# Performance work log

Measured on AMD Instinct MI355X. Metric: run time of the kernel, lower is better.

The kernel has to match this reference:

```python
import jax, jax.numpy as jnp
import numpy as np

D_MODEL = 1024
N_HEADS = 16
HEAD_DIM = D_MODEL // N_HEADS
D_FF = 4 * D_MODEL
EPS = 1e-5


def layer_norm(x, gamma, beta):
    mu = jnp.mean(x, axis=-1, keepdims=True)
    var = jnp.var(x, axis=-1, keepdims=True)
    return (x - mu) * jax.lax.rsqrt(var + EPS) * gamma + beta


def setup_inputs() -> dict:
    key = jax.random.key(0)
    ks = jax.random.split(key, 12)
    B, T, S = 4, 2048, 2048
    s_in = 1.0 / np.sqrt(D_MODEL)
    s_ff = 1.0 / np.sqrt(D_FF)
    return {
        "x": jax.random.normal(ks[0], (B, T, D_MODEL), jnp.float32),
        "context": jax.random.normal(ks[1], (B, S, D_MODEL), jnp.float32),
        "Wq": jax.random.normal(ks[2], (D_MODEL, D_MODEL), jnp.float32) * s_in,
        "Wk": jax.random.normal(ks[3], (D_MODEL, D_MODEL), jnp.float32) * s_in,
        "Wv": jax.random.normal(ks[4], (D_MODEL, D_MODEL), jnp.float32) * s_in,
        "Wo": jax.random.normal(ks[5], (D_MODEL, D_MODEL), jnp.float32) * s_in,
        "W1": jax.random.normal(ks[6], (D_FF, D_MODEL), jnp.float32) * s_in,
        "W2": jax.random.normal(ks[7], (D_MODEL, D_FF), jnp.float32) * s_ff,
        "g1": jnp.ones((D_MODEL,), jnp.float32),
        "b1": jnp.zeros((D_MODEL,), jnp.float32),
        "gc": jnp.ones((D_MODEL,), jnp.float32),
        "bc": jnp.zeros((D_MODEL,), jnp.float32),
        "g2": jnp.ones((D_MODEL,), jnp.float32),
        "b2": jnp.zeros((D_MODEL,), jnp.float32),
    }


def reference(x, context, Wq, Wk, Wv, Wo, W1, W2, g1, b1, gc, bc, g2, b2):
    B, T, C = x.shape
    S = context.shape[1]
    residual = x
    xn = layer_norm(x, g1, b1)
    cn = layer_norm(context, gc, bc)
    # torch Linear: y = x @ W.T ; split heads -> [B, H, T, Dh]
    q = (xn @ Wq.T).reshape(B, T, N_HEADS, HEAD_DIM).transpose(0, 2, 1, 3)
    k = (cn @ Wk.T).reshape(B, S, N_HEADS, HEAD_DIM).transpose(0, 2, 1, 3)
    v = (cn @ Wv.T).reshape(B, S, N_HEADS, HEAD_DIM).transpose(0, 2, 1, 3)
    scale = HEAD_DIM ** (-0.5)
    attn = jax.nn.softmax(jnp.einsum('bhtd,bhsd->bhts', q, k) * scale, axis=-1)
    o = jnp.einsum('bhts,bhsd->bhtd', attn, v).transpose(0, 2, 1, 3).reshape(B, T, C)
    x = residual + o @ Wo.T
    residual = x
    h = layer_norm(x, g2, b2)
    h = jax.nn.gelu(h @ W1.T, approximate=False) @ W2.T
    return residual + h
```

## Files before the change

### kernel.cpp

```cpp
#include <hip/hip_runtime.h>
#include <cstdint>
#include <cstddef>

typedef __attribute__((ext_vector_type(8))) short short8;
typedef __attribute__((ext_vector_type(4))) short short4v;
typedef __attribute__((ext_vector_type(4))) float f32x4;
typedef __attribute__((ext_vector_type(4))) unsigned uint4v;

#define DEV static __device__ __forceinline__

DEV short f2bf(float f) {
    unsigned u = __builtin_bit_cast(unsigned, f);
    unsigned r = (u + 0x7fffu + ((u >> 16) & 1u)) >> 16;
    return (short)r;
}

DEV unsigned cvt_pk_bf16(float a, float b) {
    unsigned r;
    asm("v_cvt_pk_bf16_f32 %0, %1, %2" : "=v"(r) : "v"(a), "v"(b));
    return r;
}

DEV float exp2_hw(float x) {
    float r;
    asm("v_exp_f32 %0, %1" : "=v"(r) : "v"(x));
    return r;
}

DEV float rcp_hw(float x) {
    float r;
    asm("v_rcp_f32 %0, %1" : "=v"(r) : "v"(x));
    return r;
}

DEV float gelu_f(float v) {
    float t  = v * (1.0f + 0.044715f * v * v);
    float e  = exp2_hw(fminf(2.3022082f * t, 126.0f));
    return v * e * rcp_hw(e + 1.0f);
}

DEV void gld16(const void* g, void* l) {
    __builtin_amdgcn_global_load_lds((const __attribute__((address_space(1))) void*)g,
                                     (__attribute__((address_space(3))) void*)l, 16, 0, 0);
}

#define MFMA(c, a, b) asm volatile("v_mfma_f32_16x16x32_bf16 %0, %1, %2, %0" : "+v"(c) : "v"(a), "v"(b))
#define BAR() asm volatile("s_barrier" ::: "memory")

__global__ __launch_bounds__(256) void cvt_weights(
    const float* __restrict__ wq, const float* __restrict__ wk,
    const float* __restrict__ wv, const float* __restrict__ wo,
    const float* __restrict__ w1, const float* __restrict__ w2,
    short* __restrict__ dst) {
    long long gid = (long long)blockIdx.x * 256 + threadIdx.x;
    long long i4 = gid * 4;
    const float* src; long long loc;
    if (i4 < (4LL << 20)) {
        int s = (int)(i4 >> 20);
        src = (s == 0) ? wq : (s == 1) ? wk : (s == 2) ? wv : wo;
        loc = i4 & ((1LL << 20) - 1);
    } else {
        long long r = i4 - (4LL << 20);
        int s = (int)(r >> 22);
        src = s ? w2 : w1;
        loc = r & ((1LL << 22) - 1);
    }
    float4 v = *(const float4*)(src + loc);
    short4v o;
    o.x = f2bf(v.x); o.y = f2bf(v.y); o.z = f2bf(v.z); o.w = f2bf(v.w);
    *(short4v*)(dst + i4) = o;
}

__global__ __launch_bounds__(256) void ln_bf16(const float* __restrict__ x,
                                               const float* __restrict__ g,
                                               const float* __restrict__ bt,
                                               short* __restrict__ out) {
    int row = blockIdx.x;
    const float4* xr = (const float4*)(x + (size_t)row * 1024);
    float4 v = xr[threadIdx.x];
    float s  = v.x + v.y + v.z + v.w;
    float s2 = v.x*v.x + v.y*v.y + v.z*v.z + v.w*v.w;
    #pragma unroll
    for (int m = 1; m < 64; m <<= 1) { s += __shfl_xor(s, m); s2 += __shfl_xor(s2, m); }
    __shared__ float red[8];
    int wid = threadIdx.x >> 6;
    if ((threadIdx.x & 63) == 0) { red[wid] = s; red[4 + wid] = s2; }
    __syncthreads();
    s  = red[0] + red[1] + red[2] + red[3];
    s2 = red[4] + red[5] + red[6] + red[7];
    float mu  = s * (1.0f / 1024.0f);
    float var = fmaxf(s2 * (1.0f / 1024.0f) - mu * mu, 0.0f);
    float rs  = rsqrtf(var + 1e-5f);
    float4 gv = ((const float4*)g)[threadIdx.x];
    float4 bv = ((const float4*)bt)[threadIdx.x];
    short4v o;
    o.x = f2bf((v.x - mu) * rs * gv.x + bv.x);
    o.y = f2bf((v.y - mu) * rs * gv.y + bv.y);
    o.z = f2bf((v.z - mu) * rs * gv.z + bv.z);
    o.w = f2bf((v.w - mu) * rs * gv.w + bv.w);
    *(short4v*)(out + (size_t)row * 1024 + (size_t)threadIdx.x * 4) = o;
}

template<int MODE>
DEV void gemm_core(const short* __restrict__ A, const short* __restrict__ B,
                   void* __restrict__ out, const float* __restrict__ resid,
                   int N, int K, int lda, int ldb, float osc, int bm, int bn) {
    __shared__ short lds[2 * 32768];
    const int tid = threadIdx.x;
    const int row0 = bm << 8, col0 = bn << 8;
    const int wid = tid >> 6, lane = tid & 63;
    const int wm = wid >> 2, wn = wid & 3;
    const int lr = lane & 15, lg = lane >> 4;
    const int NK = K >> 6;

    auto stage = [&](int kt, int which) {
        int d = kt & 1;
        const short* src; int rb; int ld;
        if (which < 2) { src = A; rb = row0; ld = lda; } else { src = B; rb = col0; ld = ldb; }
        int rhalf = (which & 1) << 7;
        short* dst = lds + d * 32768 + which * 8192;
        #pragma unroll
        for (int l = 0; l < 2; ++l) {
            int g = l * 512 + tid;
            int r = g >> 3, c = g & 7;
            gld16(src + (size_t)(rb + rhalf + r) * ld + kt * 64 + ((c ^ (r & 7)) << 3),
                  dst + g * 8);
        }
    };

    f32x4 acc[8][4] = {};

    stage(0, 0); stage(0, 1); stage(0, 2); stage(0, 3);
    if (NK > 1) {
        stage(1, 2); stage(1, 3);
        asm volatile("s_waitcnt vmcnt(4)" ::: "memory");
    } else {
        asm volatile("s_waitcnt vmcnt(0)" ::: "memory");
    }
    BAR();

    const int rBbase = (wn & 1) << 6;
    for (int t = 0; t < NK; ++t) {
        const short* bufA = lds + (t & 1) * 32768 + wm * 8192;
        const short* bufB = lds + (t & 1) * 32768 + 16384 + (wn >> 1) * 8192;
        bool st1 = (t + 1) < NK, st2 = (t + 2) < NK;
        short8 bf2[2][4];

        {
            short8 af[4];
            #pragma unroll
            for (int i = 0; i < 4; ++i) {
                int r = i * 16 + lr;
                af[i] = *(const short8*)(bufA + r * 64 + ((lg ^ (r & 7)) << 3));
            }
            #pragma unroll
            for (int j = 0; j < 4; ++j) {
                int rB = rBbase + j * 16 + lr;
                bf2[0][j] = *(const short8*)(bufB + rB * 64 + ((lg ^ (rB & 7)) << 3));
            }
            if (st1) stage(t + 1, 0);
            BAR();
            __builtin_amdgcn_s_setprio(1);
            #pragma unroll
            for (int i = 0; i < 4; ++i)
                #pragma unroll
                for (int j = 0; j < 4; ++j)
                    MFMA(acc[i][j], af[i], bf2[0][j]);
            __builtin_amdgcn_s_setprio(0);
            BAR();
        }
        {
            short8 af[4];
            #pragma unroll
            for (int i = 0; i < 4; ++i) {
                int r = i * 16 + lr;
                af[i] = *(const short8*)(bufA + r * 64 + (((4 + lg) ^ (r & 7)) << 3));
            }
            #pragma unroll
            for (int j = 0; j < 4; ++j) {
                int rB = rBbase + j * 16 + lr;
                bf2[1][j] = *(const short8*)(bufB + rB * 64 + (((4 + lg) ^ (rB & 7)) << 3));
            }
            if (st1) stage(t + 1, 1);
            BAR();
            __builtin_amdgcn_s_setprio(1);
            #pragma unroll
            for (int i = 0; i < 4; ++i)
                #pragma unroll
                for (int j = 0; j < 4; ++j)
                    MFMA(acc[i][j], af[i], bf2[1][j]);
            __builtin_amdgcn_s_setprio(0);
            BAR();
        }
        {
            short8 af[4];
            #pragma unroll
            for (int i = 0; i < 4; ++i) {
                int r = 64 + i * 16 + lr;
                af[i] = *(const short8*)(bufA + r * 64 + ((lg ^ (r & 7)) << 3));
            }
            if (st2) stage(t + 2, 2);
            BAR();
            __builtin_amdgcn_s_setprio(1);
            #pragma unroll
            for (int i = 0; i < 4; ++i)
                #pragma unroll
                for (int j = 0; j < 4; ++j)
                    MFMA(acc[4 + i][j], af[i], bf2[0][j]);
            __builtin_amdgcn_s_setprio(0);
            BAR();
        }
        {
            short8 af[4];
            #pragma unroll
            for (int i = 0; i < 4; ++i) {
                int r = 64 + i * 16 + lr;
                af[i] = *(const short8*)(bufA + r * 64 + (((4 + lg) ^ (r & 7)) << 3));
            }
            if (st2) stage(t + 2, 3);
            BAR();
            __builtin_amdgcn_s_setprio(1);
            #pragma unroll
            for (int i = 0; i < 4; ++i)
                #pragma unroll
                for (int j = 0; j < 4; ++j)
                    MFMA(acc[4 + i][j], af[i], bf2[1][j]);
            __builtin_amdgcn_s_setprio(0);
            if (st2)      asm volatile("s_waitcnt vmcnt(4)" ::: "memory");
            else if (st1) asm volatile("s_waitcnt vmcnt(0)" ::: "memory");
            BAR();
        }
    }
    asm volatile("s_nop 7\n\ts_nop 7");

    int orow0 = row0 + wm * 128, ocol0 = col0 + wn * 64;
    #pragma unroll
    for (int i = 0; i < 8; ++i)
        #pragma unroll
        for (int j = 0; j < 4; ++j)
            #pragma unroll
            for (int r = 0; r < 4; ++r) {
                int gr = orow0 + i * 16 + lg * 4 + r;
                int gc = ocol0 + j * 16 + lr;
                size_t off = (size_t)gr * N + gc;
                float v = acc[i][j][r];
                if constexpr (MODE == 1) {
                    ((float*)out)[off] = resid ? v + resid[off] : v;
                } else if constexpr (MODE == 2) {
                    ((short*)out)[off] = f2bf(gelu_f(v));
                } else {
                    ((short*)out)[off] = f2bf(v * osc);
                }
            }
}

__global__ __launch_bounds__(512, 2) void gemm_qkv(
    const short* __restrict__ XN, const short* __restrict__ CN,
    const short* __restrict__ Wq, const short* __restrict__ Wk, const short* __restrict__ Wv,
    short* __restrict__ QB, short* __restrict__ KB, short* __restrict__ VT, float qscale) {
    int sid = (blockIdx.x & 7) * 48 + (blockIdx.x >> 3);
    int sub = sid >> 7, i = sid & 127;
    const short *A, *B; short* o; float osc; int N, bm, bn;
    if (sub == 0)      { A = XN; B = Wq; o = QB; osc = qscale; N = 1024; bm = i >> 2; bn = i & 3; }
    else if (sub == 1) { A = CN; B = Wk; o = KB; osc = 1.0f;   N = 1024; bm = i >> 2; bn = i & 3; }
    else               { A = Wv; B = CN; o = VT; osc = 1.0f;   N = 8192; bm = i >> 5; bn = i & 31; }
    gemm_core<3>(A, B, o, nullptr, N, 1024, 1024, 1024, osc, bm, bn);
}

template<int MODE>
__global__ __launch_bounds__(512, 2) void gemm_std(const short* __restrict__ A,
                                                   const short* __restrict__ B,
                                                   void* __restrict__ out,
                                                   const float* __restrict__ resid,
                                                   int N, int K, float osc) {
    int cpx = gridDim.x >> 3;
    int sid = (blockIdx.x & 7) * cpx + (blockIdx.x >> 3);
    int nbn = N >> 8;
    int bm = sid / nbn, bn = sid % nbn;
    gemm_core<MODE>(A, B, out, resid, N, K, K, K, osc, bm, bn);
}

__global__ __launch_bounds__(512, 2) void gemm_ff2(const short* __restrict__ F1,
                                                   const short* __restrict__ W2,
                                                   float* __restrict__ dOut,
                                                   float* __restrict__ P2,
                                                   const float* __restrict__ X2) {
    int sid = (blockIdx.x & 7) * 32 + (blockIdx.x >> 3);
    int h = sid >> 7, i = sid & 127;
    int bm = i >> 2, bn = i & 3;
    const short* A = F1 + h * 2048;
    const short* B = W2 + h * 2048;
    float* o = h ? P2 : dOut;
    const float* r = h ? nullptr : X2;
    gemm_core<1>(A, B, o, r, 1024, 2048, 4096, 4096, 1.0f, bm, bn);
}

__global__ __launch_bounds__(256) void add_f32(float* __restrict__ dst,
                                               const float* __restrict__ src, int n4) {
    int i = blockIdx.x * 256 + threadIdx.x;
    int stride = gridDim.x * 256;
    for (; i < n4; i += stride) {
        float4 a = ((const float4*)dst)[i];
        float4 b = ((const float4*)src)[i];
        a.x += b.x; a.y += b.y; a.z += b.z; a.w += b.w;
        ((float4*)dst)[i] = a;
    }
}

__global__ __launch_bounds__(512, 6) void attn(const short* __restrict__ Q,
                                               const short* __restrict__ K,
                                               const short* __restrict__ Vt,
                                               short* __restrict__ O) {
    __shared__ short lK[2][64 * 64];
    __shared__ short lV[2][64 * 64];
    int tid = threadIdx.x;
    int sid = (blockIdx.x & 7) * 128 + (blockIdx.x >> 3);
    int bh = sid >> 4, qt = sid & 15;
    int b = bh >> 4, h = bh & 15;
    int wid = tid >> 6, lane = tid & 63;
    int lr = lane & 15, lg = lane >> 4;
    int q0 = qt * 128 + wid * 16;
    bool cbit = (lane & 16) != 0;
    bool hihalf = (lane & 32) != 0;

    short8 qf[2];
    #pragma unroll
    for (int kb = 0; kb < 2; ++kb) {
        size_t roff = (size_t)(b * 2048 + q0 + lr) * 1024 + h * 64 + kb * 32 + lg * 8;
        qf[kb] = *(const short8*)(Q + roff);
    }

    f32x4 oacc[4] = {};
    float mrow = -1e30f, lsum = 0.0f;

    const short* Kb = K + (size_t)(b * 2048) * 1024 + h * 64;
    const short* Vb = Vt + (size_t)(h * 64) * 8192 + b * 2048;
    int albase = (lane & 48) >> 2;

    int sr = tid >> 3, scc = tid & 7;
    int ssl = scc ^ (sr & 7);
    auto stage = [&](int st, int d) {
        gld16(Kb + (size_t)(st * 64 + sr) * 1024 + ssl * 8, &lK[d][tid * 8]);
        gld16(Vb + (size_t)sr * 8192 + st * 64 + ssl * 8, &lV[d][tid * 8]);
    };

    stage(0, 0);
    asm volatile("s_waitcnt vmcnt(0)" ::: "memory");
    BAR();

    for (int st = 0; st < 32; ++st) {
        int d = st & 1;
        if (st + 1 < 32) stage(st + 1, d ^ 1);

        f32x4 sc2[4] = {};
        #pragma unroll
        for (int kb = 0; kb < 2; ++kb) {
            short8 kf[4];
            #pragma unroll
            for (int fn = 0; fn < 4; ++fn) {
                int kr = fn * 16 + lr;
                kf[fn] = *(const short8*)(lK[d] + kr * 64 + (((kb * 4 + lg) ^ (kr & 7)) << 3));
            }
            #pragma unroll
            for (int fn = 0; fn < 4; ++fn)
                MFMA(sc2[fn], kf[fn], qf[kb]);
        }
        asm volatile("s_nop 7\n\ts_nop 7");

        float pm = sc2[0][0];
        #pragma unroll
        for (int fn = 0; fn < 4; ++fn)
            #pragma unroll
            for (int r = 0; r < 4; ++r)
                if (fn | r) pm = fmaxf(pm, sc2[fn][r]);
        pm = fmaxf(pm, __shfl_xor(pm, 16));
        pm = fmaxf(pm, __shfl_xor(pm, 32));

        float al = 1.0f;
        float mn = mrow;
        if (!__all(pm <= mrow + 8.0f)) {
            mn = fmaxf(mrow, pm);
            al = exp2_hw(mrow - mn);
            mrow = mn;
            #pragma unroll
            for (int r = 0; r < 4; ++r) {
                float alr = __shfl(al, albase + r);
                #pragma unroll
                for (int fn = 0; fn < 4; ++fn) oacc[fn][r] *= alr;
            }
        }

        float p[4][4];
        float ps = 0.0f;
        #pragma unroll
        for (int fn = 0; fn < 4; ++fn)
            #pragma unroll
            for (int r = 0; r < 4; ++r) {
                p[fn][r] = exp2_hw(sc2[fn][r] - mn);
                ps += p[fn][r];
            }
        ps += __shfl_xor(ps, 16);
        ps += __shfl_xor(ps, 32);
        lsum = lsum * al + ps;

        unsigned U[4][2];
        #pragma unroll
        for (int fn = 0; fn < 4; ++fn) {
            U[fn][0] = cvt_pk_bf16(p[fn][0], p[fn][1]);
            U[fn][1] = cvt_pk_bf16(p[fn][2], p[fn][3]);
        }

        #pragma unroll
        for (int kb = 0; kb < 2; ++kb) {
            unsigned lo0 = U[kb * 2][0],     lo1 = U[kb * 2][1];
            unsigned hi0 = U[kb * 2 + 1][0], hi1 = U[kb * 2 + 1][1];
            unsigned t0 = (unsigned)__shfl_xor((int)lo0, 32);
            unsigned t1 = (unsigned)__shfl_xor((int)lo1, 32);
            unsigned s0 = (unsigned)__shfl_xor((int)hi0, 32);
            unsigned s1 = (unsigned)__shfl_xor((int)hi1, 32);
            unsigned nlo0 = hihalf ? s0 : lo0;
            unsigned nlo1 = hihalf ? s1 : lo1;
            unsigned nhi0 = hihalf ? hi0 : t0;
            unsigned nhi1 = hihalf ? hi1 : t1;
            unsigned a0 = cbit ? nhi0 : nlo0;
            unsigned a1 = cbit ? nhi1 : nlo1;
            unsigned x0 = (unsigned)__shfl_xor((int)nlo0, 16);
            unsigned x1 = (unsigned)__shfl_xor((int)nlo1, 16);
            unsigned y0 = (unsigned)__shfl_xor((int)nhi0, 16);
            unsigned y1 = (unsigned)__shfl_xor((int)nhi1, 16);
            unsigned b0 = cbit ? y0 : x0;
            unsigned b1 = cbit ? y1 : x1;
            uint4v pw;
            pw.x = cbit ? b0 : a0;
            pw.y = cbit ? b1 : a1;
            pw.z = cbit ? a0 : b0;
            pw.w = cbit ? a1 : b1;
            short8 pa = __builtin_bit_cast(short8, pw);

            short8 vf[4];
            #pragma unroll
            for (int fn = 0; fn < 4; ++fn) {
                int vr = fn * 16 + lr;
                vf[fn] = *(const short8*)(lV[d] + vr * 64 + (((kb * 4 + lg) ^ (vr & 7)) << 3));
            }
            #pragma unroll
            for (int fn = 0; fn < 4; ++fn)
                MFMA(oacc[fn], pa, vf[fn]);
        }

        asm volatile("s_waitcnt vmcnt(0)" ::: "memory");
        BAR();
    }
    asm volatile("s_nop 7\n\ts_nop 7");

    #pragma unroll
    for (int r = 0; r < 4; ++r) {
        float linv = __shfl(lsum, albase + r);
        float inv = 1.0f / linv;
        #pragma unroll
        for (int fn = 0; fn < 4; ++fn) {
            size_t off = (size_t)(b * 2048 + q0 + lg * 4 + r) * 1024 + h * 64 + fn * 16 + lr;
            O[off] = f2bf(oacc[fn][r] * inv);
        }
    }
}

extern "C" void kernel_launch(void* const* d_in, const int* in_sizes, int n_in,
                              void* d_out, int out_size, void* d_ws, size_t ws_size,
                              hipStream_t stream) {
    const float* x   = (const float*)d_in[0];
    const float* ctx = (const float*)d_in[1];
    const float* Wq  = (const float*)d_in[2];
    const float* Wk  = (const float*)d_in[3];
    const float* Wv  = (const float*)d_in[4];
    const float* Wo  = (const float*)d_in[5];
    const float* W1  = (const float*)d_in[6];
    const float* W2  = (const float*)d_in[7];
    const float* g1  = (const float*)d_in[8];
    const float* b1  = (const float*)d_in[9];
    const float* gc  = (const float*)d_in[10];
    const float* bc  = (const float*)d_in[11];
    const float* g2  = (const float*)d_in[12];
    const float* b2  = (const float*)d_in[13];

    char* ws = (char*)d_ws;
    const size_t OFF_W  = 0;
    const size_t OFF_XN = 25165824;
    const size_t OFF_CN = OFF_XN + 16777216;
    const size_t OFF_QB = OFF_CN + 16777216;
    const size_t OFF_KB = OFF_QB + 16777216;
    const size_t OFF_VT = OFF_KB + 16777216;
    const size_t OFF_X2 = OFF_VT + 16777216;
    const size_t OFF_F1 = OFF_X2 + 33554432;

    short* Wb = (short*)(ws + OFF_W);
    short* XN = (short*)(ws + OFF_XN);
    short* CN = (short*)(ws + OFF_CN);
    short* QB = (short*)(ws + OFF_QB);
    short* KB = (short*)(ws + OFF_KB);
    short* VT = (short*)(ws + OFF_VT);
    float* X2 = (float*)(ws + OFF_X2);
    short* F1 = (short*)(ws + OFF_F1);
    short* OB = XN;
    short* H  = CN;
    float* P2 = (float*)(ws + OFF_QB);

    const size_t WQo = 0, WKo = 1048576, WVo = 2097152, WOo = 3145728;
    const size_t W1o = 4194304, W2o = 8388608;
    const float QSCALE = 0.125f * 1.4426950408889634f;

    cvt_weights<<<12288, 256, 0, stream>>>(Wq, Wk, Wv, Wo, W1, W2, Wb);
    ln_bf16<<<8192, 256, 0, stream>>>(x, g1, b1, XN);
    ln_bf16<<<8192, 256, 0, stream>>>(ctx, gc, bc, CN);
    gemm_qkv<<<384, 512, 0, stream>>>(XN, CN, Wb + WQo, Wb + WKo, Wb + WVo, QB, KB, VT, QSCALE);
    attn<<<1024, 512, 0, stream>>>(QB, KB, VT, OB);
    gemm_std<1><<<128, 512, 0, stream>>>(OB, Wb + WOo, X2, x, 1024, 1024, 1.0f);
    ln_bf16<<<8192, 256, 0, stream>>>(X2, g2, b2, H);
    gemm_std<2><<<512, 512, 0, stream>>>(H, Wb + W1o, F1, nullptr, 4096, 1024, 1.0f);
    gemm_ff2<<<256, 512, 0, stream>>>(F1, Wb + W2o, (float*)d_out, P2, X2);
    add_f32<<<2048, 256, 0, stream>>>((float*)d_out, P2, 2097152);
}
```

Baseline: 467.4 us.

## Remove P-fragment shuffles by permuting V LDS reads; use permlane32 swap reductions

```diff
diff --git a/kernel.cpp b/kernel.cpp
--- a/kernel.cpp
+++ b/kernel.cpp
@@ -46,6 +46,17 @@
 
 #define MFMA(c, a, b) asm volatile("v_mfma_f32_16x16x32_bf16 %0, %1, %2, %0" : "+v"(c) : "v"(a), "v"(b))
 #define BAR() asm volatile("s_barrier" ::: "memory")
+
+DEV float red32_max(float v) {
+    float a = v, b = v;
+    asm volatile("v_permlane32_swap_b32 %0, %1" : "+v"(a), "+v"(b));
+    return fmaxf(a, b);
+}
+DEV float red32_add(float v) {
+    float a = v, b = v;
+    asm volatile("v_permlane32_swap_b32 %0, %1" : "+v"(a), "+v"(b));
+    return a + b;
+}
 
 __global__ __launch_bounds__(256) void cvt_weights(
     const float* __restrict__ wq, const float* __restrict__ wk,
@@ -320,8 +331,6 @@
     int wid = tid >> 6, lane = tid & 63;
     int lr = lane & 15, lg = lane >> 4;
     int q0 = qt * 128 + wid * 16;
-    bool cbit = (lane & 16) != 0;
-    bool hihalf = (lane & 32) != 0;
 
     short8 qf[2];
     #pragma unroll
@@ -367,14 +376,15 @@
         }
         asm volatile("s_nop 7\n\ts_nop 7");
 
-        float pm = sc2[0][0];
-        #pragma unroll
-        for (int fn = 0; fn < 4; ++fn)
-            #pragma unroll
-            for (int r = 0; r < 4; ++r)
-                if (fn | r) pm = fmaxf(pm, sc2[fn][r]);
+        float m8[8];
+        #pragma unroll
+        for (int i = 0; i < 8; ++i)
+            m8[i] = fmaxf(sc2[i >> 2][i & 3], sc2[(i + 8) >> 2][(i + 8) & 3]);
+        float ma = fmaxf(fmaxf(m8[0], m8[1]), fmaxf(m8[2], m8[3]));
+        float mb = fmaxf(fmaxf(m8[4], m8[5]), fmaxf(m8[6], m8[7]));
+        float pm = fmaxf(ma, mb);
         pm = fmaxf(pm, __shfl_xor(pm, 16));
-        pm = fmaxf(pm, __shfl_xor(pm, 32));
+        pm = red32_max(pm);
 
         float al = 1.0f;
         float mn = mrow;
@@ -391,16 +401,20 @@
         }
 
         float p[4][4];
-        float ps = 0.0f;
         #pragma unroll
         for (int fn = 0; fn < 4; ++fn)
             #pragma unroll
-            for (int r = 0; r < 4; ++r) {
+            for (int r = 0; r < 4; ++r)
                 p[fn][r] = exp2_hw(sc2[fn][r] - mn);
-                ps += p[fn][r];
-            }
+        float s8[8];
+        #pragma unroll
+        for (int i = 0; i < 8; ++i)
+            s8[i] = p[i >> 2][i & 3] + p[(i + 8) >> 2][(i + 8) & 3];
+        float sa = (s8[0] + s8[1]) + (s8[2] + s8[3]);
+        float sb = (s8[4] + s8[5]) + (s8[6] + s8[7]);
+        float ps = sa + sb;
         ps += __shfl_xor(ps, 16);
-        ps += __shfl_xor(ps, 32);
+        ps = red32_add(ps);
         lsum = lsum * al + ps;
 
         unsigned U[4][2];
@@ -412,40 +426,23 @@
 
         #pragma unroll
         for (int kb = 0; kb < 2; ++kb) {
-            unsigned lo0 = U[kb * 2][0],     lo1 = U[kb * 2][1];
-            unsigned hi0 = U[kb * 2 + 1][0], hi1 = U[kb * 2 + 1][1];
-            unsigned t0 = (unsigned)__shfl_xor((int)lo0, 32);
-            unsigned t1 = (unsigned)__shfl_xor((int)lo1, 32);
-            unsigned s0 = (unsigned)__shfl_xor((int)hi0, 32);
-            unsigned s1 = (unsigned)__shfl_xor((int)hi1, 32);
-            unsigned nlo0 = hihalf ? s0 : lo0;
-            unsigned nlo1 = hihalf ? s1 : lo1;
-            unsigned nhi0 = hihalf ? hi0 : t0;
-            unsigned nhi1 = hihalf ? hi1 : t1;
-            unsigned a0 = cbit ? nhi0 : nlo0;
-            unsigned a1 = cbit ? nhi1 : nlo1;
-            unsigned x0 = (unsigned)__shfl_xor((int)nlo0, 16);
-            unsigned x1 = (unsigned)__shfl_xor((int)nlo1, 16);
-            unsigned y0 = (unsigned)__shfl_xor((int)nhi0, 16);
-            unsigned y1 = (unsigned)__shfl_xor((int)nhi1, 16);
-            unsigned b0 = cbit ? y0 : x0;
-            unsigned b1 = cbit ? y1 : x1;
             uint4v pw;
-            pw.x = cbit ? b0 : a0;
-            pw.y = cbit ? b1 : a1;
-            pw.z = cbit ? a0 : b0;
-            pw.w = cbit ? a1 : b1;
+            pw.x = U[kb * 2][0];
+            pw.y = U[kb * 2][1];
+            pw.z = U[kb * 2 + 1][0];
+            pw.w = U[kb * 2 + 1][1];
             short8 pa = __builtin_bit_cast(short8, pw);
 
-            short8 vf[4];
             #pragma unroll
             for (int fn = 0; fn < 4; ++fn) {
                 int vr = fn * 16 + lr;
-                vf[fn] = *(const short8*)(lV[d] + vr * 64 + (((kb * 4 + lg) ^ (vr & 7)) << 3));
-            }
-            #pragma unroll
-            for (int fn = 0; fn < 4; ++fn)
-                MFMA(oacc[fn], pa, vf[fn]);
+                int so_lo = (((kb * 4 + (lg >> 1)) ^ (vr & 7)) << 3) + ((lg & 1) << 2);
+                int so_hi = (((kb * 4 + 2 + (lg >> 1)) ^ (vr & 7)) << 3) + ((lg & 1) << 2);
+                union { short4v h[2]; short8 v; } u;
+                u.h[0] = *(const short4v*)(lV[d] + vr * 64 + so_lo);
+                u.h[1] = *(const short4v*)(lV[d] + vr * 64 + so_hi);
+                MFMA(oacc[fn], pa, u.v);
+            }
         }
 
         asm volatile("s_waitcnt vmcnt(0)" ::: "memory");
```

Measured after the change: 453.5 us. 3.0% less time.
